# Kernel tuning notes

Measured on AMD Instinct MI355X. Metric: run time of the kernel, lower is better.

Reference implementation:

```python
import jax, jax.numpy as jnp
import numpy as np

N_NODES = 100000
N_GRAPHS = 128

def _graph_conv(x, W, b, s, d, n_nodes):
    """DGL GraphConv with norm='both': D_dst^{-1/2} A D_src^{-1/2} X W + b."""
    ones = jnp.ones(s.shape[0], x.dtype)
    deg_out = jax.ops.segment_sum(ones, s, num_segments=n_nodes)  # src out-degree
    deg_in = jax.ops.segment_sum(ones, d, num_segments=n_nodes)   # dst in-degree
    norm_src = jnp.where(deg_out > 0, 1.0 / jnp.sqrt(jnp.maximum(deg_out, 1.0)), 0.0)
    norm_dst = jnp.where(deg_in > 0, 1.0 / jnp.sqrt(jnp.maximum(deg_in, 1.0)), 0.0)
    h = x * norm_src[:, None]                    # [N, F]
    agg = jax.ops.segment_sum(h[s], d, num_segments=n_nodes)  # SpMM gather-scatter
    rst = (agg @ W) * norm_dst[:, None] + b
    return rst

def _hetero_layer(x, Ws, bs, src, dst, n_nodes):
    # HeteroGraphConv aggregate='sum' over relations (fixed small set -> loop ok)
    out = jnp.zeros((n_nodes, Ws.shape[-1]), x.dtype)
    for r in range(Ws.shape[0]):
        out = out + _graph_conv(x, Ws[r], bs[r], src[r], dst[r], n_nodes)
    return out

def setup_inputs() -> dict:
    key = jax.random.key(0)
    ks = jax.random.split(key, 8)
    feat = jax.random.normal(ks[0], (N_NODES, 256), dtype=jnp.float32)
    src = jax.random.randint(ks[1], (3, 400000), 0, N_NODES)
    dst = jax.random.randint(ks[2], (3, 400000), 0, N_NODES)
    graph_ids = jnp.sort(jax.random.randint(ks[3], (N_NODES,), 0, N_GRAPHS))
    W1 = jax.random.normal(ks[4], (3, 256, 256), dtype=jnp.float32) * 0.06
    b1 = jnp.zeros((3, 256), dtype=jnp.float32)
    W2 = jax.random.normal(ks[5], (3, 256, 256), dtype=jnp.float32) * 0.06
    b2 = jnp.zeros((3, 256), dtype=jnp.float32)
    return {"feat": feat, "src": src, "dst": dst, "graph_ids": graph_ids,
            "W1": W1, "b1": b1, "W2": W2, "b2": b2}

def reference(feat, src, dst, graph_ids, W1, b1, W2, b2):
    n_nodes = feat.shape[0]
    h = _hetero_layer(feat, W1, b1, src, dst, n_nodes)
    h = jax.nn.relu(h)
    h = _hetero_layer(h, W2, b2, src, dst, n_nodes)
    # AvgPooling over batched graphs
    sums = jax.ops.segment_sum(h, graph_ids, num_segments=N_GRAPHS)
    counts = jax.ops.segment_sum(jnp.ones(n_nodes, h.dtype), graph_ids, num_segments=N_GRAPHS)
    return sums / jnp.maximum(counts, 1.0)[:, None]
```

## Files before the change

kernel.cpp:

```cpp
#include <hip/hip_runtime.h>
#include <stdint.h>

#define NN 100000
#define NE 400000
#define NR 3
#define NF 256
#define NK 768
#define NG 128
#define SCAN_NB ((NN + 1023) / 1024)

typedef __attribute__((ext_vector_type(4))) unsigned short ushortx4;
typedef __attribute__((ext_vector_type(8))) short short8;
typedef __attribute__((ext_vector_type(4))) float floatx4;

static __device__ __forceinline__ unsigned short f2bfu(float f) {
  union { float f; uint32_t u; } c; c.f = f;
  uint32_t x = c.u;
  uint32_t r = (x + 0x7fffu + ((x >> 16) & 1u)) >> 16;
  return (unsigned short)r;
}
static __device__ __forceinline__ float bfu2f(unsigned short u) {
  union { uint32_t u; float f; } c; c.u = ((uint32_t)u) << 16;
  return c.f;
}

static __device__ __forceinline__ void gload16(const void* g, void* l) {
  __builtin_amdgcn_global_load_lds(
      (const __attribute__((address_space(1))) uint32_t*)g,
      (__attribute__((address_space(3))) uint32_t*)l, 16, 0, 0);
}


__global__ __launch_bounds__(256) void degree_kernel(
    const int* __restrict__ src, const int* __restrict__ dst,
    int* __restrict__ deg_out, int* __restrict__ deg_in) {
  int t = blockIdx.x * 256 + threadIdx.x;
  int r = blockIdx.y;
  if (t < NE) {
    atomicAdd(&deg_out[r * NN + src[r * NE + t]], 1);
    atomicAdd(&deg_in[r * NN + dst[r * NE + t]], 1);
  }
}

__global__ __launch_bounds__(128) void gcount_kernel(
    const int* __restrict__ gid, int* __restrict__ gcount) {
  int g = threadIdx.x;
  int lo = 0, hi = NN;
  while (lo < hi) { int mid = (lo + hi) >> 1; if (gid[mid] < g) lo = mid + 1; else hi = mid; }
  int a = lo;
  lo = 0; hi = NN;
  while (lo < hi) { int mid = (lo + hi) >> 1; if (gid[mid] < g + 1) lo = mid + 1; else hi = mid; }
  gcount[g] = lo - a;
}

__global__ __launch_bounds__(256) void norm_kernel(
    const int* __restrict__ deg_out, const int* __restrict__ deg_in,
    float* __restrict__ n_src, float* __restrict__ n_dst) {
  int t = blockIdx.x * 256 + threadIdx.x;
  if (t < NR * NN) {
    int dof = deg_out[t], din = deg_in[t];
    n_src[t] = dof > 0 ? rsqrtf((float)dof) : 0.f;
    n_dst[t] = din > 0 ? rsqrtf((float)din) : 0.f;
  }
}


__global__ __launch_bounds__(256) void scan_phaseA(
    const int* __restrict__ deg_in, int* __restrict__ blocksum) {
  int r = blockIdx.y, b = blockIdx.x, tid = threadIdx.x;
  const int* deg = deg_in + (size_t)r * NN;
  int base = b * 1024 + tid * 4;
  int s = 0;
#pragma unroll
  for (int i = 0; i < 4; ++i) { int idx = base + i; if (idx < NN) s += deg[idx]; }
  __shared__ int red[256];
  red[tid] = s; __syncthreads();
  for (int off = 128; off > 0; off >>= 1) {
    if (tid < off) red[tid] += red[tid + off];
    __syncthreads();
  }
  if (tid == 0) blocksum[r * SCAN_NB + b] = red[0];
}

__global__ __launch_bounds__(128) void scan_phaseB(
    int* __restrict__ blocksum, int* __restrict__ rowptr) {
  int r = blockIdx.x, tid = threadIdx.x;
  int* bs = blocksum + r * SCAN_NB;
  __shared__ int buf[128];
  int v = (tid < SCAN_NB) ? bs[tid] : 0;
  buf[tid] = v; __syncthreads();
  for (int off = 1; off < 128; off <<= 1) {
    int t = (tid >= off) ? buf[tid - off] : 0;
    __syncthreads();
    buf[tid] += t;
    __syncthreads();
  }
  if (tid < SCAN_NB) bs[tid] = buf[tid] - v;
  if (tid == 127) rowptr[(size_t)r * (NN + 1) + NN] = buf[127];
}

__global__ __launch_bounds__(256) void scan_phaseC(
    const int* __restrict__ deg_in, const int* __restrict__ blocksum,
    int* __restrict__ rowptr) {
  int r = blockIdx.y, b = blockIdx.x, tid = threadIdx.x;
  const int* deg = deg_in + (size_t)r * NN;
  int* rp = rowptr + (size_t)r * (NN + 1);
  int base = b * 1024 + tid * 4;
  int v[4]; int s = 0;
#pragma unroll
  for (int i = 0; i < 4; ++i) { int idx = base + i; v[i] = (idx < NN) ? deg[idx] : 0; s += v[i]; }
  __shared__ int buf[256];
  buf[tid] = s; __syncthreads();
  for (int off = 1; off < 256; off <<= 1) {
    int t = (tid >= off) ? buf[tid - off] : 0;
    __syncthreads();
    buf[tid] += t;
    __syncthreads();
  }
  int excl = buf[tid] - s + blocksum[r * SCAN_NB + b];
#pragma unroll
  for (int i = 0; i < 4; ++i) {
    int idx = base + i;
    if (idx < NN) rp[idx] = excl;
    excl += v[i];
  }
}

__global__ __launch_bounds__(256) void scatter_kernel(
    const int* __restrict__ src, const int* __restrict__ dst,
    const int* __restrict__ rowptr, int* __restrict__ cursor,
    const float* __restrict__ n_src,
    int* __restrict__ csr_src, float* __restrict__ csr_w) {
  int t = blockIdx.x * 256 + threadIdx.x;
  int r = blockIdx.y;
  if (t < NE) {
    int s = src[r * NE + t], v = dst[r * NE + t];
    int pos = atomicAdd(&cursor[r * NN + v], 1);
    int idx = r * NE + rowptr[(size_t)r * (NN + 1) + v] + pos;
    csr_src[idx] = s;
    csr_w[idx] = n_src[r * NN + s];
  }
}


__global__ __launch_bounds__(256) void prep_w_kernel(
    const float* __restrict__ W1, const float* __restrict__ W2,
    unsigned short* __restrict__ wt1, unsigned short* __restrict__ wt2) {
  int t = blockIdx.x * 256 + threadIdx.x;
  int lay = t / (NR * NF * NF);
  int rem = t % (NR * NF * NF);
  int r = rem / (NF * NF);
  int k = (rem / NF) % NF;
  int n = rem % NF;
  const float* W = lay ? W2 : W1;
  unsigned short* wt = lay ? wt2 : wt1;
  wt[(size_t)n * NK + r * NF + k] = f2bfu(W[((size_t)r * NF + k) * NF + n]);
}

__global__ __launch_bounds__(256) void prep_bias_kernel(
    const float* __restrict__ b1, const float* __restrict__ b2,
    float* __restrict__ bs1, float* __restrict__ bs2) {
  int t = blockIdx.x * 256 + threadIdx.x;
  if (t < 2 * NF) {
    int lay = t / NF, n = t % NF;
    const float* b = lay ? b2 : b1;
    float* bs = lay ? bs2 : bs1;
    bs[n] = b[n] + b[NF + n] + b[2 * NF + n];
  }
}

__global__ __launch_bounds__(256) void cast_kernel(
    const float* __restrict__ in, unsigned short* __restrict__ out, int n4) {
  int t = blockIdx.x * 256 + threadIdx.x;
  if (t < n4) {
    floatx4 v = *(const floatx4*)&in[(size_t)t * 4];
    ushortx4 o;
    o.x = f2bfu(v.x); o.y = f2bfu(v.y); o.z = f2bfu(v.z); o.w = f2bfu(v.w);
    *(ushortx4*)&out[(size_t)t * 4] = o;
  }
}


__global__ __launch_bounds__(256) void spmm_kernel(
    const unsigned short* __restrict__ x,
    const int* __restrict__ rowptr, const int* __restrict__ csr_src,
    const float* __restrict__ csr_w, const float* __restrict__ n_dst,
    unsigned short* __restrict__ agg) {
  int wid = threadIdx.x >> 6, l = threadIdx.x & 63;
  int r = blockIdx.y;
  int v = blockIdx.x * 4 + wid;
  if (v >= NN) return;
  int e0 = rowptr[(size_t)r * (NN + 1) + v];
  int e1 = rowptr[(size_t)r * (NN + 1) + v + 1];
  const int* cs = csr_src + (size_t)r * NE;
  const float* cw = csr_w + (size_t)r * NE;
  float a0 = 0.f, a1 = 0.f, a2 = 0.f, a3 = 0.f;
  int e = e0;
  for (; e + 4 <= e1; e += 4) {
    int s0 = cs[e], s1 = cs[e + 1], s2 = cs[e + 2], s3 = cs[e + 3];
    float w0 = cw[e], w1 = cw[e + 1], w2 = cw[e + 2], w3 = cw[e + 3];
    ushortx4 x0 = *(const ushortx4*)&x[(size_t)s0 * NF + l * 4];
    ushortx4 x1 = *(const ushortx4*)&x[(size_t)s1 * NF + l * 4];
    ushortx4 x2 = *(const ushortx4*)&x[(size_t)s2 * NF + l * 4];
    ushortx4 x3 = *(const ushortx4*)&x[(size_t)s3 * NF + l * 4];
    a0 += w0 * bfu2f(x0.x) + w1 * bfu2f(x1.x) + w2 * bfu2f(x2.x) + w3 * bfu2f(x3.x);
    a1 += w0 * bfu2f(x0.y) + w1 * bfu2f(x1.y) + w2 * bfu2f(x2.y) + w3 * bfu2f(x3.y);
    a2 += w0 * bfu2f(x0.z) + w1 * bfu2f(x1.z) + w2 * bfu2f(x2.z) + w3 * bfu2f(x3.z);
    a3 += w0 * bfu2f(x0.w) + w1 * bfu2f(x1.w) + w2 * bfu2f(x2.w) + w3 * bfu2f(x3.w);
  }
  for (; e < e1; ++e) {
    int s = cs[e];
    float w = cw[e];
    ushortx4 xv = *(const ushortx4*)&x[(size_t)s * NF + l * 4];
    a0 += w * bfu2f(xv.x);
    a1 += w * bfu2f(xv.y);
    a2 += w * bfu2f(xv.z);
    a3 += w * bfu2f(xv.w);
  }
  float nd = n_dst[r * NN + v];
  ushortx4 o;
  o.x = f2bfu(a0 * nd); o.y = f2bfu(a1 * nd);
  o.z = f2bfu(a2 * nd); o.w = f2bfu(a3 * nd);
  *(ushortx4*)&agg[(size_t)v * NK + r * NF + l * 4] = o;
}


__global__ __launch_bounds__(256, 2) void gemm_kernel(
    const unsigned short* __restrict__ A,
    const unsigned short* __restrict__ Bt,
    const float* __restrict__ bias,
    unsigned short* __restrict__ C,
    int M, int relu) {
  __shared__ unsigned short ldsA[128 * 32];
  __shared__ unsigned short ldsB[256 * 32];
  const int tid = threadIdx.x;
  const int l = tid & 63, wid = tid >> 6;
  const int row0 = blockIdx.x * 128;
  const int c0 = wid * 64;

  floatx4 acc[8][4];
#pragma unroll
  for (int i = 0; i < 8; ++i)
#pragma unroll
    for (int j = 0; j < 4; ++j)
#pragma unroll
      for (int q = 0; q < 4; ++q) acc[i][j][q] = 0.f;

  const int fr = l & 15, fk = (l >> 4) * 8;

  for (int kt = 0; kt < NK / 32; ++kt) {
    const int k0 = kt * 32;
    {
      int u = wid * 64 + l;
      int arow = row0 + (u >> 2);
      if (arow >= M) arow = M - 1;
      gload16(A + (size_t)arow * NK + k0 + (u & 3) * 8, &ldsA[u * 8]);
      u += 256;
      arow = row0 + (u >> 2);
      if (arow >= M) arow = M - 1;
      gload16(A + (size_t)arow * NK + k0 + (u & 3) * 8, &ldsA[u * 8]);
    }
#pragma unroll
    for (int p = 0; p < 4; ++p) {
      int u = p * 256 + wid * 64 + l;
      int col = u >> 2;
      gload16(Bt + (size_t)col * NK + k0 + (u & 3) * 8, &ldsB[u * 8]);
    }
    asm volatile("s_waitcnt vmcnt(0)" ::: "memory");
    __syncthreads();

    short8 af[8], bf[4];
#pragma unroll
    for (int m = 0; m < 8; ++m)
      af[m] = *(const short8*)&ldsA[(m * 16 + fr) * 32 + fk];
#pragma unroll
    for (int n = 0; n < 4; ++n)
      bf[n] = *(const short8*)&ldsB[(c0 + n * 16 + fr) * 32 + fk];
#pragma unroll
    for (int m = 0; m < 8; ++m)
#pragma unroll
      for (int n = 0; n < 4; ++n)
        acc[m][n] = __builtin_amdgcn_mfma_f32_16x16x32_bf16(af[m], bf[n], acc[m][n], 0, 0, 0);
    __syncthreads();
  }

  const int fq = l >> 4;
#pragma unroll
  for (int m = 0; m < 8; ++m) {
#pragma unroll
    for (int n = 0; n < 4; ++n) {
      int col = c0 + n * 16 + fr;
      float bv = bias[col];
#pragma unroll
      for (int q = 0; q < 4; ++q) {
        int row = row0 + m * 16 + fq * 4 + q;
        if (row < M) {
          float vv = acc[m][n][q] + bv;
          if (relu) vv = fmaxf(vv, 0.f);
          C[(size_t)row * NF + col] = f2bfu(vv);
        }
      }
    }
  }
}


__global__ __launch_bounds__(256) void pool_kernel(
    const unsigned short* __restrict__ h2, const int* __restrict__ gid,
    float* __restrict__ poolsum) {
  int c = threadIdx.x;
  int v0 = blockIdx.x * 256;
  int vend = min(v0 + 256, NN);
  float acc = 0.f;
  int curg = -1;
  for (int v = v0; v < vend; ++v) {
    int g = gid[v];
    if (g != curg) {
      if (curg >= 0) atomicAdd(&poolsum[curg * NF + c], acc);
      curg = g; acc = 0.f;
    }
    acc += bfu2f(h2[(size_t)v * NF + c]);
  }
  if (curg >= 0) atomicAdd(&poolsum[curg * NF + c], acc);
}

__global__ __launch_bounds__(256) void final_kernel(
    const float* __restrict__ poolsum, const int* __restrict__ gcount,
    float* __restrict__ out) {
  int g = blockIdx.x, c = threadIdx.x;
  out[g * NF + c] = poolsum[g * NF + c] / fmaxf((float)gcount[g], 1.f);
}


extern "C" void kernel_launch(void* const* d_in, const int* in_sizes, int n_in,
                              void* d_out, int out_size, void* d_ws, size_t ws_size,
                              hipStream_t stream) {
  const float* feat = (const float*)d_in[0];
  const int* src = (const int*)d_in[1];
  const int* dst = (const int*)d_in[2];
  const int* gid = (const int*)d_in[3];
  const float* W1 = (const float*)d_in[4];
  const float* b1 = (const float*)d_in[5];
  const float* W2 = (const float*)d_in[6];
  const float* b2 = (const float*)d_in[7];
  float* out = (float*)d_out;

  char* ws = (char*)d_ws;
  size_t off = 0;
  auto alloc = [&](size_t bytes) -> void* {
    void* p = ws + off;
    off = (off + bytes + 255) & ~(size_t)255;
    return p;
  };

  int* deg_out = (int*)alloc((size_t)NR * NN * 4);
  int* deg_in  = (int*)alloc((size_t)NR * NN * 4);
  int* cursor  = (int*)alloc((size_t)NR * NN * 4);
  float* poolsum = (float*)alloc((size_t)NG * NF * 4);
  size_t zero_bytes = off;

  int* gcount  = (int*)alloc((size_t)NG * 4);
  int* blocksum = (int*)alloc((size_t)NR * SCAN_NB * 4);
  float* n_src = (float*)alloc((size_t)NR * NN * 4);
  float* n_dst = (float*)alloc((size_t)NR * NN * 4);
  int* rowptr  = (int*)alloc((size_t)NR * (NN + 1) * 4);
  int* csr_src = (int*)alloc((size_t)NR * NE * 4);
  float* csr_w = (float*)alloc((size_t)NR * NE * 4);
  unsigned short* wt1 = (unsigned short*)alloc((size_t)NF * NK * 2);
  unsigned short* wt2 = (unsigned short*)alloc((size_t)NF * NK * 2);
  float* bs1 = (float*)alloc(NF * 4);
  float* bs2 = (float*)alloc(NF * 4);
  unsigned short* featbf = (unsigned short*)alloc((size_t)NN * NF * 2);
  unsigned short* h1 = (unsigned short*)alloc((size_t)NN * NF * 2);
  unsigned short* h2 = (unsigned short*)alloc((size_t)NN * NF * 2);
  unsigned short* agg = (unsigned short*)alloc((size_t)NN * NK * 2);
  (void)ws_size; (void)in_sizes; (void)n_in; (void)out_size;

  hipMemsetAsync(d_ws, 0, zero_bytes, stream);

  dim3 eg((NE + 255) / 256, NR);
  degree_kernel<<<eg, 256, 0, stream>>>(src, dst, deg_out, deg_in);
  gcount_kernel<<<1, 128, 0, stream>>>(gid, gcount);
  norm_kernel<<<(NR * NN + 255) / 256, 256, 0, stream>>>(deg_out, deg_in, n_src, n_dst);
  scan_phaseA<<<dim3(SCAN_NB, NR), 256, 0, stream>>>(deg_in, blocksum);
  scan_phaseB<<<NR, 128, 0, stream>>>(blocksum, rowptr);
  scan_phaseC<<<dim3(SCAN_NB, NR), 256, 0, stream>>>(deg_in, blocksum, rowptr);
  scatter_kernel<<<eg, 256, 0, stream>>>(src, dst, rowptr, cursor, n_src, csr_src, csr_w);

  prep_w_kernel<<<(2 * NR * NF * NF) / 256, 256, 0, stream>>>(W1, W2, wt1, wt2);
  prep_bias_kernel<<<2, 256, 0, stream>>>(b1, b2, bs1, bs2);
  cast_kernel<<<(NN * NF / 4 + 255) / 256, 256, 0, stream>>>(feat, featbf, NN * NF / 4);

  dim3 sg((NN + 3) / 4, NR);
  spmm_kernel<<<sg, 256, 0, stream>>>(featbf, rowptr, csr_src, csr_w, n_dst, agg);
  gemm_kernel<<<(NN + 127) / 128, 256, 0, stream>>>(agg, wt1, bs1, h1, NN, 1);
  spmm_kernel<<<sg, 256, 0, stream>>>(h1, rowptr, csr_src, csr_w, n_dst, agg);
  gemm_kernel<<<(NN + 127) / 128, 256, 0, stream>>>(agg, wt2, bs2, h2, NN, 0);
  pool_kernel<<<(NN + 255) / 256, 256, 0, stream>>>(h2, gid, poolsum);
  final_kernel<<<NG, 256, 0, stream>>>(poolsum, gcount, out);
}
```

Before: 740.0 us.

## Pack CSR src/weight into int2 and split SpMM wave into half-waves over edges

Scatter now writes the source index and normalisation weight as one interleaved int2 per edge, so SpMM fetches both with a single 8-byte load. The SpMM kernel has each half of the 64-lane wave handle alternating edges with 16-byte (8 bf16) feature loads, then combines the halves with a cross-half shuffle before the store. This aims to cut the number of memory instructions and raise bytes per load in the gather-bound SpMM. The cost is an extra shuffle reduction per row, and the tail loop masks out-of-range lanes by loading row 0 with zero weight.

```diff
diff --git a/kernel.cpp b/kernel.cpp
--- a/kernel.cpp
+++ b/kernel.cpp
@@ -10,6 +10,7 @@
 #define SCAN_NB ((NN + 1023) / 1024)
 
 typedef __attribute__((ext_vector_type(4))) unsigned short ushortx4;
+typedef __attribute__((ext_vector_type(8))) unsigned short ushortx8;
 typedef __attribute__((ext_vector_type(8))) short short8;
 typedef __attribute__((ext_vector_type(4))) float floatx4;
 
@@ -130,15 +131,14 @@
     const int* __restrict__ src, const int* __restrict__ dst,
     const int* __restrict__ rowptr, int* __restrict__ cursor,
     const float* __restrict__ n_src,
-    int* __restrict__ csr_src, float* __restrict__ csr_w) {
+    int2* __restrict__ csr_e) {
   int t = blockIdx.x * 256 + threadIdx.x;
   int r = blockIdx.y;
   if (t < NE) {
     int s = src[r * NE + t], v = dst[r * NE + t];
     int pos = atomicAdd(&cursor[r * NN + v], 1);
     int idx = r * NE + rowptr[(size_t)r * (NN + 1) + v] + pos;
-    csr_src[idx] = s;
-    csr_w[idx] = n_src[r * NN + s];
+    csr_e[idx] = make_int2(s, __float_as_int(n_src[r * NN + s]));
   }
 }
 
@@ -183,8 +183,8 @@
 
 __global__ __launch_bounds__(256) void spmm_kernel(
     const unsigned short* __restrict__ x,
-    const int* __restrict__ rowptr, const int* __restrict__ csr_src,
-    const float* __restrict__ csr_w, const float* __restrict__ n_dst,
+    const int* __restrict__ rowptr, const int2* __restrict__ csr_e,
+    const float* __restrict__ n_dst,
     unsigned short* __restrict__ agg) {
   int wid = threadIdx.x >> 6, l = threadIdx.x & 63;
   int r = blockIdx.y;
@@ -192,36 +192,44 @@
   if (v >= NN) return;
   int e0 = rowptr[(size_t)r * (NN + 1) + v];
   int e1 = rowptr[(size_t)r * (NN + 1) + v + 1];
-  const int* cs = csr_src + (size_t)r * NE;
-  const float* cw = csr_w + (size_t)r * NE;
-  float a0 = 0.f, a1 = 0.f, a2 = 0.f, a3 = 0.f;
+  const int2* ce = csr_e + (size_t)r * NE;
+  const int half = l >> 5;
+  const int c8 = (l & 31) * 8;
+
+  float a[8];
+#pragma unroll
+  for (int j = 0; j < 8; ++j) a[j] = 0.f;
+
   int e = e0;
   for (; e + 4 <= e1; e += 4) {
-    int s0 = cs[e], s1 = cs[e + 1], s2 = cs[e + 2], s3 = cs[e + 3];
-    float w0 = cw[e], w1 = cw[e + 1], w2 = cw[e + 2], w3 = cw[e + 3];
-    ushortx4 x0 = *(const ushortx4*)&x[(size_t)s0 * NF + l * 4];
-    ushortx4 x1 = *(const ushortx4*)&x[(size_t)s1 * NF + l * 4];
-    ushortx4 x2 = *(const ushortx4*)&x[(size_t)s2 * NF + l * 4];
-    ushortx4 x3 = *(const ushortx4*)&x[(size_t)s3 * NF + l * 4];
-    a0 += w0 * bfu2f(x0.x) + w1 * bfu2f(x1.x) + w2 * bfu2f(x2.x) + w3 * bfu2f(x3.x);
-    a1 += w0 * bfu2f(x0.y) + w1 * bfu2f(x1.y) + w2 * bfu2f(x2.y) + w3 * bfu2f(x3.y);
-    a2 += w0 * bfu2f(x0.z) + w1 * bfu2f(x1.z) + w2 * bfu2f(x2.z) + w3 * bfu2f(x3.z);
-    a3 += w0 * bfu2f(x0.w) + w1 * bfu2f(x1.w) + w2 * bfu2f(x2.w) + w3 * bfu2f(x3.w);
-  }
-  for (; e < e1; ++e) {
-    int s = cs[e];
-    float w = cw[e];
-    ushortx4 xv = *(const ushortx4*)&x[(size_t)s * NF + l * 4];
-    a0 += w * bfu2f(xv.x);
-    a1 += w * bfu2f(xv.y);
-    a2 += w * bfu2f(xv.z);
-    a3 += w * bfu2f(xv.w);
-  }
-  float nd = n_dst[r * NN + v];
-  ushortx4 o;
-  o.x = f2bfu(a0 * nd); o.y = f2bfu(a1 * nd);
-  o.z = f2bfu(a2 * nd); o.w = f2bfu(a3 * nd);
-  *(ushortx4*)&agg[(size_t)v * NK + r * NF + l * 4] = o;
+    int2 p0 = ce[e + half];
+    int2 p1 = ce[e + 2 + half];
+    float w0 = __int_as_float(p0.y), w1 = __int_as_float(p1.y);
+    ushortx8 x0 = *(const ushortx8*)&x[(size_t)p0.x * NF + c8];
+    ushortx8 x1 = *(const ushortx8*)&x[(size_t)p1.x * NF + c8];
+#pragma unroll
+    for (int j = 0; j < 8; ++j) a[j] += w0 * bfu2f(x0[j]) + w1 * bfu2f(x1[j]);
+  }
+  for (; e < e1; e += 2) {
+    int idx = e + half;
+    bool ok = idx < e1;
+    int2 p = ok ? ce[idx] : make_int2(0, 0);
+    float w = ok ? __int_as_float(p.y) : 0.f;
+    ushortx8 xv = *(const ushortx8*)&x[(size_t)p.x * NF + c8];
+#pragma unroll
+    for (int j = 0; j < 8; ++j) a[j] += w * bfu2f(xv[j]);
+  }
+
+#pragma unroll
+  for (int j = 0; j < 8; ++j) a[j] += __shfl_xor(a[j], 32);
+
+  if (l < 32) {
+    float nd = n_dst[r * NN + v];
+    ushortx8 o;
+#pragma unroll
+    for (int j = 0; j < 8; ++j) o[j] = f2bfu(a[j] * nd);
+    *(ushortx8*)&agg[(size_t)v * NK + r * NF + c8] = o;
+  }
 }
 
 
@@ -364,8 +372,7 @@
   float* n_src = (float*)alloc((size_t)NR * NN * 4);
   float* n_dst = (float*)alloc((size_t)NR * NN * 4);
   int* rowptr  = (int*)alloc((size_t)NR * (NN + 1) * 4);
-  int* csr_src = (int*)alloc((size_t)NR * NE * 4);
-  float* csr_w = (float*)alloc((size_t)NR * NE * 4);
+  int2* csr_e  = (int2*)alloc((size_t)NR * NE * 8);
   unsigned short* wt1 = (unsigned short*)alloc((size_t)NF * NK * 2);
   unsigned short* wt2 = (unsigned short*)alloc((size_t)NF * NK * 2);
   float* bs1 = (float*)alloc(NF * 4);
@@ -385,16 +392,16 @@
   scan_phaseA<<<dim3(SCAN_NB, NR), 256, 0, stream>>>(deg_in, blocksum);
   scan_phaseB<<<NR, 128, 0, stream>>>(blocksum, rowptr);
   scan_phaseC<<<dim3(SCAN_NB, NR), 256, 0, stream>>>(deg_in, blocksum, rowptr);
-  scatter_kernel<<<eg, 256, 0, stream>>>(src, dst, rowptr, cursor, n_src, csr_src, csr_w);
+  scatter_kernel<<<eg, 256, 0, stream>>>(src, dst, rowptr, cursor, n_src, csr_e);
 
   prep_w_kernel<<<(2 * NR * NF * NF) / 256, 256, 0, stream>>>(W1, W2, wt1, wt2);
   prep_bias_kernel<<<2, 256, 0, stream>>>(b1, b2, bs1, bs2);
   cast_kernel<<<(NN * NF / 4 + 255) / 256, 256, 0, stream>>>(feat, featbf, NN * NF / 4);
 
   dim3 sg((NN + 3) / 4, NR);
-  spmm_kernel<<<sg, 256, 0, stream>>>(featbf, rowptr, csr_src, csr_w, n_dst, agg);
+  spmm_kernel<<<sg, 256, 0, stream>>>(featbf, rowptr, csr_e, n_dst, agg);
   gemm_kernel<<<(NN + 127) / 128, 256, 0, stream>>>(agg, wt1, bs1, h1, NN, 1);
-  spmm_kernel<<<sg, 256, 0, stream>>>(h1, rowptr, csr_src, csr_w, n_dst, agg);
+  spmm_kernel<<<sg, 256, 0, stream>>>(h1, rowptr, csr_e, n_dst, agg);
   gemm_kernel<<<(NN + 127) / 128, 256, 0, stream>>>(agg, wt2, bs2, h2, NN, 0);
   pool_kernel<<<(NN + 255) / 256, 256, 0, stream>>>(h2, gid, poolsum);
   final_kernel<<<NG, 256, 0, stream>>>(poolsum, gcount, out);
```

Measured after the change: 718.4 us. -2.9%, faster.
